# Kernel optimization log

Measured on AMD Instinct MI355X. Metric: run time of the kernel, lower is better.

## Reference

```python
import jax, jax.numpy as jnp
import numpy as np
from math import factorial, sqrt, pi

MUL = 8
LS = [0, 1, 2]                       # l values for both Rs_in and Rs_out
RS = [(MUL, l) for l in LS]
N_NODES = 20000
N_EDGES = 100000
FEAT = sum(m * (2 * l + 1) for m, l in RS)       # 72
R_TOT = sum(mo * mi * (2 * min(lo, li) + 1) for mo, lo in RS for mi, li in RS)  # 1216
L_MAX = max(LS) + max(LS)            # 4
RSH_DIM = (L_MAX + 1) ** 2           # 25
NB, H = 10, 100                      # radial basis size / hidden width
MIN_R, MAX_R = 0.7, 3.2
SWISH_SCALE = 1.679177               # e3nn rescaled swish factor


def _w3j_entry(j1, j2, j3, m1, m2, m3):
    # complex-basis Wigner 3j (Racah formula)
    if m1 + m2 + m3 != 0 or not (abs(j1 - j2) <= j3 <= j1 + j2):
        return 0.0
    t1, t2 = j2 - m1 - j3, j1 + m2 - j3
    kmin, kmax = max(0, t1, t2), min(j1 + j2 - j3, j1 - m1, j2 + m2)
    s = sum((-1) ** k / (factorial(k) * factorial(k - t1) * factorial(k - t2)
                         * factorial(j1 + j2 - j3 - k) * factorial(j1 - m1 - k) * factorial(j2 + m2 - k))
            for k in range(kmin, kmax + 1))
    pref = (-1) ** (j1 - j2 - m3) * sqrt(
        factorial(j1 + j2 - j3) * factorial(j1 - j2 + j3) * factorial(-j1 + j2 + j3) / factorial(j1 + j2 + j3 + 1)
        * factorial(j1 + m1) * factorial(j1 - m1) * factorial(j2 + m2) * factorial(j2 - m2)
        * factorial(j3 + m3) * factorial(j3 - m3))
    return pref * s


def _real_cob(l):
    # complex->real spherical-harmonic change of basis
    U = np.zeros((2 * l + 1, 2 * l + 1), dtype=complex)
    U[l, l] = 1.0
    s = 1.0 / np.sqrt(2.0)
    for m in range(1, l + 1):
        U[l + m, l + m] = (-1) ** m * s
        U[l + m, l - m] = s
        U[l - m, l - m] = 1j * s
        U[l - m, l + m] = -1j * ((-1) ** m) * s
    return U


def _wigner3j_real(l1, l2, l3):
    w = np.zeros((2 * l1 + 1, 2 * l2 + 1, 2 * l3 + 1))
    for m1 in range(-l1, l1 + 1):
        for m2 in range(-l2, l2 + 1):
            m3 = -m1 - m2
            if abs(m3) <= l3:
                w[m1 + l1, m2 + l2, m3 + l3] = _w3j_entry(l1, l2, l3, m1, m2, m3)
    T = np.einsum('am,bn,cp,mnp->abc', _real_cob(l1), _real_cob(l2), _real_cob(l3), w.astype(complex))
    C = T.real if np.linalg.norm(T.real) >= np.linalg.norm(T.imag) else T.imag
    n = np.linalg.norm(C)
    return (C / n if n > 0 else C).astype(np.float32)


# precomputed constants (coupling coefficients + normalization), as in MinimalNetwork.__init__
C3 = {(lo, li, lf): jnp.asarray(_wigner3j_real(lo, li, lf))
      for _, lo in RS for _, li in RS for lf in range(abs(lo - li), lo + li + 1)}


def _norm_coef():
    nc = np.zeros((len(RS), len(RS)), dtype=np.float32)
    for i, (_, lo) in enumerate(RS):
        num = sum(mi * (2 * min(lo, li) + 1) for mi, li in RS)
        nc[i, :] = sqrt(4 * pi) * sqrt(2 * lo + 1) / sqrt(num)
    return jnp.asarray(nc)

NORM = _norm_coef()


def _swish(x):
    return SWISH_SCALE * x * jax.nn.sigmoid(x)


def _radial(r, Ws):
    # GaussianRadialModel: gaussian basis -> 3 hidden swish layers -> linear out
    centers = jnp.linspace(MIN_R, MAX_R, NB)
    sigma = (MAX_R - MIN_R) / (NB - 1)
    x = jnp.exp(-(((r[:, None] - centers) / sigma) ** 2))
    for W in Ws[:-1]:
        x = _swish(x @ (W / jnp.sqrt(jnp.asarray(W.shape[0], x.dtype))))
    W = Ws[-1]
    return x @ (W / jnp.sqrt(jnp.asarray(W.shape[0], x.dtype)))


def _tensor_message(F_src, rsh, R):
    # F_src: [E, FEAT] gathered source features; rsh: [E, 25]; R: [E, R_TOT]
    E = F_src.shape[0]
    f_offs = np.cumsum([0] + [m * (2 * l + 1) for m, l in RS])
    msgs, r_off = [], 0
    for i, (U, lo) in enumerate(RS):
        acc = jnp.zeros((E, U, 2 * lo + 1), F_src.dtype)
        for j, (V, li) in enumerate(RS):
            nlf = 2 * min(lo, li) + 1
            Rb = R[:, r_off:r_off + U * V * nlf].reshape(E, U, V, nlf)
            r_off += U * V * nlf
            Fb = F_src[:, f_offs[j]:f_offs[j + 1]].reshape(E, V, 2 * li + 1)
            for fi, lf in enumerate(range(abs(lo - li), lo + li + 1)):
                # K[e,mo,mi] = sum_mf C3[mo,mi,mf] * Y_lf[e,mf]
                K = jnp.einsum('oif,ef->eoi', C3[(lo, li, lf)], rsh[:, lf * lf:(lf + 1) * (lf + 1)])
                acc = acc + NORM[i, j] * jnp.einsum('eoi,evi,euv->euo', K, Fb, Rb[..., fi])
        msgs.append(acc.reshape(E, -1))
    return jnp.concatenate(msgs, axis=-1)


def _forward(features, edge_index, radii, rsh, Ws):
    R = _radial(radii, Ws)                                     # [E, R_TOT]
    msg = _tensor_message(features[edge_index[0]], rsh, R)     # [E, FEAT]
    # scatter-add aggregation at target nodes (MessagePassing aggr='add')
    return jnp.zeros((features.shape[0], msg.shape[1]), msg.dtype).at[edge_index[1]].add(msg)


def setup_inputs() -> dict:
    key = jax.random.key(0)
    ks = jax.random.split(key, 8)
    features = jax.random.normal(ks[0], (N_NODES, FEAT), jnp.float32)
    edge_index = jax.random.randint(ks[1], (2, N_EDGES), 0, N_NODES)
    radii = MIN_R + (MAX_R - MIN_R) * jax.random.uniform(ks[2], (N_EDGES,), jnp.float32)
    rsh = jax.random.normal(ks[3], (N_EDGES, RSH_DIM), jnp.float32)
    W0 = jax.random.normal(ks[4], (NB, H), jnp.float32)
    W1 = jax.random.normal(ks[5], (H, H), jnp.float32)
    W2 = jax.random.normal(ks[6], (H, H), jnp.float32)
    W3 = jax.random.normal(ks[7], (H, R_TOT), jnp.float32)
    return {"features": features, "edge_index": edge_index, "radii": radii, "rsh": rsh,
            "W0": W0, "W1": W1, "W2": W2, "W3": W3}


def reference(features, edge_index, radii, rsh, W0, W1, W2, W3):
    return _forward(features, edge_index, radii, rsh, (W0, W1, W2, W3))
```

## Files before the change

### kernel.cpp

```cpp
#include <hip/hip_runtime.h>
#include <hip/hip_bf16.h>
#include <math.h>


#define FEATD 72
#define NCOL 1216
#define SWISH_SCALE 1.679177f

typedef __attribute__((ext_vector_type(8))) short bf16x8;
typedef __attribute__((ext_vector_type(4))) float f32x4;

constexpr int NCOMBO = 19;
constexpr int CB_LO[NCOMBO] = {0,0,0,1,1,1,1,1,1,1,2,2,2,2,2,2,2,2,2};
constexpr int CB_LI[NCOMBO] = {0,1,2,0,1,1,1,2,2,2,0,1,1,1,2,2,2,2,2};
constexpr int CB_LF[NCOMBO] = {0,1,2,1,0,1,2,1,2,3,2,1,2,3,0,1,2,3,4};
constexpr int CB_OFF[NCOMBO] = {0,1,10,35,44,53,80,125,170,245,350,375,420,495,600,625,700,825,1000};
constexpr int CB_SZ[NCOMBO]  = {1,9,25,9,9,27,45,45,75,105,25,45,75,105,25,75,125,175,225};
constexpr int C3TOT = 1225;

constexpr int C3OFFT[3][3][5] = {
  { {0,-1,-1,-1,-1}, {-1,1,-1,-1,-1}, {-1,-1,10,-1,-1} },
  { {-1,35,-1,-1,-1}, {44,53,80,-1,-1}, {-1,125,170,245,-1} },
  { {-1,-1,350,-1,-1}, {-1,375,420,495,-1}, {600,625,700,825,1000} }
};
constexpr int ROFFT[3][3] = {{0,64,128},{192,256,448},{640,704,896}};
constexpr int FOFFT[3]   = {0,8,32};

__device__ const double d_fact[11] = {1.,1.,2.,6.,24.,120.,720.,5040.,40320.,362880.,3628800.};

__device__ double w3j_entry(int j1,int j2,int j3,int m1,int m2,int m3){
  if (m1+m2+m3 != 0) return 0.0;
  int dj = j1-j2; if (dj<0) dj=-dj;
  if (j3 < dj || j3 > j1+j2) return 0.0;
  int t1 = j2 - m1 - j3, t2 = j1 + m2 - j3;
  int kmin = 0; if (t1>kmin) kmin=t1; if (t2>kmin) kmin=t2;
  int kmax = j1+j2-j3; if (j1-m1<kmax) kmax=j1-m1; if (j2+m2<kmax) kmax=j2+m2;
  double s = 0.0;
  for (int k=kmin;k<=kmax;++k){
    double den = d_fact[k]*d_fact[k-t1]*d_fact[k-t2]*d_fact[j1+j2-j3-k]
               * d_fact[j1-m1-k]*d_fact[j2+m2-k];
    s += ((k&1)? -1.0:1.0)/den;
  }
  double pref = sqrt(d_fact[j1+j2-j3]*d_fact[j1-j2+j3]*d_fact[-j1+j2+j3]/d_fact[j1+j2+j3+1]
               * d_fact[j1+m1]*d_fact[j1-m1]*d_fact[j2+m2]*d_fact[j2-m2]
               * d_fact[j3+m3]*d_fact[j3-m3]);
  int ex = j1-j2-m3;
  if (ex & 1) pref = -pref;
  return pref*s;
}

__device__ void cob(int l, int r, int c, double& re, double& im){
  re = 0.0; im = 0.0;
  int mr = r - l, mc = c - l;
  const double s = 0.70710678118654752440;
  if (mr == 0) { if (mc == 0) re = 1.0; return; }
  if (mr > 0) {
    if (mc == mr)       re = (mr & 1) ? -s : s;
    else if (mc == -mr) re = s;
  } else {
    int m = -mr;
    if (mc == -m)      im = s;
    else if (mc == m)  im = (m & 1) ? s : -s;
  }
}

__global__ void c3_combined_kernel(float* __restrict__ C3f){
  __shared__ double sre[225], sim[225];
  const int c = blockIdx.x;
  const int lo = CB_LO[c], li = CB_LI[c], lf = CB_LF[c];
  const int off = CB_OFF[c], sz = CB_SZ[c];
  const int n2 = 2*li+1, n3 = 2*lf+1;
  const int t = threadIdx.x;

  for (int p=t; p<sz; p+=64){
    int a = p/(n2*n3), b = (p/n3)%n2, g = p%n3;
    double re=0.0, im=0.0;
    for (int m1=-lo; m1<=lo; ++m1){
      for (int m2=-li; m2<=li; ++m2){
        int m3 = -m1-m2;
        if (m3 < -lf || m3 > lf) continue;
        double w = w3j_entry(lo,li,lf,m1,m2,m3);
        if (w == 0.0) continue;
        double r1,i1,r2,i2,r3,i3;
        cob(lo, a, m1+lo, r1,i1);
        cob(li, b, m2+li, r2,i2);
        cob(lf, g, m3+lf, r3,i3);
        double rr = r1*r2 - i1*i2, ri = r1*i2 + i1*r2;
        double fr = rr*r3 - ri*i3, fi = rr*i3 + ri*r3;
        re += fr*w; im += fi*w;
      }
    }
    sre[p] = re; sim[p] = im;
  }
  __syncthreads();
  double s2r=0.0, s2i=0.0;
  for (int p=t; p<sz; p+=64){ double x=sre[p], y=sim[p]; s2r+=x*x; s2i+=y*y; }
  for (int m=1; m<64; m<<=1){ s2r += __shfl_xor(s2r, m, 64); s2i += __shfl_xor(s2i, m, 64); }
  bool useRe = (s2r >= s2i);
  double n = sqrt(useRe ? s2r : s2i);
  double inv = (n > 0.0) ? 1.0/n : 1.0;
  for (int p=t; p<sz; p+=64){
    double v = useRe ? sre[p] : sim[p];
    C3f[off+p] = (float)(v*inv);
  }
}

__global__ __launch_bounds__(256) void prep_combined_kernel(
    const float* __restrict__ W3, const float* __restrict__ W1,
    const float* __restrict__ W2, __hip_bfloat16* __restrict__ W3t,
    __hip_bfloat16* __restrict__ W1t, __hip_bfloat16* __restrict__ W2t)
{
  int idx = blockIdx.x*256 + threadIdx.x;
  constexpr int NW3 = 1216*128;
  constexpr int HALF = 112*128;
  if (idx < NW3){
    int cp = idx >> 7, k = idx & 127;
    int chunk = cp >> 6, r = cp & 63;
    int lo = CB_LO[chunk], li = CB_LI[chunk], lf = CB_LF[chunk];
    int lmin = lo<li ? lo : li;
    int nlf = 2*lmin+1;
    int fi = lf - (lo>li ? lo-li : li-lo);
    int c = ROFFT[lo][li] + r*nlf + fi;
    float v = (k < 100) ? 0.1f*W3[(size_t)k*NCOL + c] : 0.f;
    int swz = (r*16 + (k>>3)) ^ (r&7);
    W3t[(size_t)chunk*8192 + swz*8 + (k&7)] = __float2bfloat16(v);
  } else if (idx < NW3 + 2*HALF){
    int r2 = idx - NW3;
    const float* W = (r2 < HALF) ? W1 : W2;
    __hip_bfloat16* Wt = (r2 < HALF) ? W1t : W2t;
    int r = (r2 < HALF) ? r2 : r2 - HALF;
    int o = r >> 7, k = r & 127;
    float v = (o < 100 && k < 100) ? 0.1f*W[k*100+o] : 0.f;
    int swz = (o*16 + (k>>3)) ^ (o&7);
    Wt[swz*8 + (k&7)] = __float2bfloat16(v);
  }
}

__global__ __launch_bounds__(256) void hist_kernel(const int* __restrict__ ei,
                                                   int* __restrict__ deg, int E){
  int e = blockIdx.x*256 + threadIdx.x;
  if (e < E) atomicAdd(&deg[ei[E+e]], 1);
}

__global__ __launch_bounds__(256) void scan_kernel(const int* __restrict__ deg,
                                                   int* __restrict__ off,
                                                   int* __restrict__ cursor, int N, int E){
  __shared__ int part[256], spref[256];
  const int t = threadIdx.x;
  const int CH = (N + 255)/256;
  int lo = t*CH, hi = lo+CH < N ? lo+CH : N;
  int s = 0;
  for (int n=lo; n<hi; ++n) s += deg[n];
  part[t] = s;
  __syncthreads();
  if (t == 0){
    int run = 0;
    for (int i=0;i<256;++i){ spref[i] = run; run += part[i]; }
  }
  __syncthreads();
  int run = spref[t];
  for (int n=lo; n<hi; ++n){ off[n] = run; cursor[n] = run; run += deg[n]; }
  if (t == 255) off[N] = E;
}

__global__ __launch_bounds__(256) void fill_kernel(const int* __restrict__ ei,
                                                   int* __restrict__ cursor,
                                                   int* __restrict__ eid, int E){
  int e = blockIdx.x*256 + threadIdx.x;
  if (e < E){
    int idx = atomicAdd(&cursor[ei[E+e]], 1);
    eid[idx] = e;
  }
}

__global__ __launch_bounds__(64) void gather_kernel(const float* __restrict__ msg,
                                                    const int* __restrict__ off,
                                                    const int* __restrict__ eid,
                                                    float* __restrict__ out, int N){
  const int n = blockIdx.x;
  const int t = threadIdx.x;
  const int s = off[n], e1 = off[n+1];
  float a0 = 0.f, a1 = 0.f;
  for (int i=s; i<e1; ++i){
    const float* m = msg + (size_t)eid[i]*FEATD;
    a0 += m[t];
    if (t < 8) a1 += m[64+t];
  }
  out[(size_t)n*FEATD + t] = a0;
  if (t < 8) out[(size_t)n*FEATD + 64 + t] = a1;
}

constexpr int OF_W   = 0;
constexpr int OF_RT  = 16384;
constexpr int OF_ACC = 33792;
constexpr int OF_F   = 44032;
constexpr int OF_KV  = 63488;
constexpr int OF_C3  = 76288;
constexpr int OF_SRC = 81188;
constexpr int SMEM_SZ = 81444;

constexpr int OF_RW   = 0;
constexpr int OF_BAS  = 28672;
constexpr int OF_HA   = 31232;
constexpr int OF_HB   = 48640;

__device__ __forceinline__ float swishf(float s){
  return SWISH_SCALE * s / (1.f + __expf(-s));
}

__device__ __forceinline__ void stage_w(const __hip_bfloat16* __restrict__ Wt,
                                        char* sW, int t)
{
  const int lane = t & 63, wv = t >> 6;
  const char* g = (const char*)Wt;
  #pragma unroll
  for (int i=0; i<7; ++i){
    const char* gsrc = g + (i*256 + wv*64 + lane)*16;
    __builtin_amdgcn_global_load_lds(
        (const __attribute__((address_space(1))) unsigned int*)gsrc,
        (__attribute__((address_space(3))) unsigned int*)(sW + i*4096 + wv*1024),
        16, 0, 0);
  }
}

__device__ __forceinline__ void radial_layer_lds(
    const __hip_bfloat16* __restrict__ sIn,
    const char* __restrict__ sW,
    __hip_bfloat16* __restrict__ sOut,
    int wv, int lr, int lq)
{
  bf16x8 bf[4];
  #pragma unroll
  for (int ks=0; ks<4; ++ks)
    bf[ks] = *(const bf16x8*)&sIn[(wv*16+lr)*136 + ks*32 + lq*8];
  f32x4 acc[7] = {};
  #pragma unroll
  for (int ks=0; ks<4; ++ks)
    #pragma unroll
    for (int ot=0; ot<7; ++ot){
      const int row = ot*16 + lr;
      const int u = (row*16 + ks*4 + lq) ^ (row & 7);
      bf16x8 a = *(const bf16x8*)(sW + u*16);
      acc[ot] = __builtin_amdgcn_mfma_f32_16x16x32_bf16(a, bf[ks], acc[ot], 0, 0, 0);
    }
  #pragma unroll
  for (int ot=0; ot<7; ++ot){
    __hip_bfloat16 hv[4];
    #pragma unroll
    for (int r=0; r<4; ++r)
      hv[r] = __float2bfloat16(swishf(acc[ot][r]));
    *(short4*)&sOut[(wv*16+lr)*136 + ot*16 + lq*4] = *(short4*)hv;
  }
  {
    int lane = lq*16 + lr;
    int row = lane & 15, q = lane >> 4;
    short4 z = {0,0,0,0};
    *(short4*)&sOut[(wv*16+row)*136 + 112 + q*4] = z;
  }
}

__device__ __forceinline__ void stage_chunk(const __hip_bfloat16* __restrict__ W3t,
                                            int chunk, char* sW, int t)
{
  const int lane = t & 63, wv = t >> 6;
  const char* g = (const char*)W3t + (size_t)chunk*16384;
  #pragma unroll
  for (int r=0; r<4; ++r){
    const char* gsrc = g + (wv*256 + r*64 + lane)*16;
    __builtin_amdgcn_global_load_lds(
        (const __attribute__((address_space(1))) unsigned int*)gsrc,
        (__attribute__((address_space(3))) unsigned int*)(sW + wv*4096 + r*1024),
        16, 0, 0);
  }
}

template<int LO,int LI,int LF>
__device__ __forceinline__ void kv_sec(float* kvb, const float* sC3,
                                       const float* __restrict__ rshrow,
                                       int e, int role)
{
  constexpr int NO = 2*LO+1, NI = 2*LI+1, NF = 2*LF+1;
  constexpr int C3B = C3OFFT[LO][LI][LF];
  float y[NF];
  #pragma unroll
  for (int mf=0; mf<NF; ++mf) y[mf] = rshrow[LF*LF + mf];
  for (int it = role; it < NO*NI; it += 4){
    float s = 0.f;
    #pragma unroll
    for (int mf=0; mf<NF; ++mf) s += sC3[C3B + it*NF + mf] * y[mf];
    kvb[e*25 + it] = s;
  }
}

template<int LO,int LI>
__device__ __forceinline__ void consume_sec(
    const float* sRt, const float* sFf, const float* kvb, float* sAcc,
    int e, int role)
{
  constexpr int NO = 2*LO+1, NI = 2*LI+1;
  constexpr int FO = FOFFT[LI];
  float H[2][NI];
  #pragma unroll
  for (int du=0; du<2; ++du)
    #pragma unroll
    for (int mi=0; mi<NI; ++mi) H[du][mi] = 0.f;

  #pragma unroll
  for (int vg=0; vg<2; ++vg){
    float fb[4*NI];
    #pragma unroll
    for (int p=0; p<NI; ++p)
      *(f32x4*)&fb[p*4] = *(const f32x4*)&sFf[e*76 + FO + vg*4*NI + p*4];
    #pragma unroll
    for (int du=0; du<2; ++du){
      const int u = role*2 + du;
      f32x4 rv = *(const f32x4*)&sRt[e*68 + u*8 + vg*4];
      #pragma unroll
      for (int v=0; v<4; ++v)
        #pragma unroll
        for (int mi=0; mi<NI; ++mi)
          H[du][mi] += rv[v] * fb[v*NI + mi];
    }
  }
  const int u0 = role*2, u1 = role*2 + 1;
  const int b0 = e*40 + ((LO==0) ? u0 : (LO==1) ? u0*3 : u0*5);
  const int b1 = e*40 + ((LO==0) ? u1 : (LO==1) ? u1*3 : u1*5);
  #pragma unroll
  for (int o=0; o<NO; ++o){
    float s0 = 0.f, s1 = 0.f;
    #pragma unroll
    for (int mi=0; mi<NI; ++mi){
      float kvv = kvb[e*25 + o*NI + mi];
      s0 += kvv * H[0][mi];
      s1 += kvv * H[1][mi];
    }
    sAcc[b0 + o] += s0;
    sAcc[b1 + o] += s1;
  }
}

__device__ __forceinline__ void mfma_sec(const char* sW, float* sRt,
                                         const bf16x8 (&hf)[4],
                                         int wv, int lr, int lq)
{
  f32x4 a4[4] = {};
  #pragma unroll
  for (int ks=0; ks<4; ++ks){
    #pragma unroll
    for (int ct=0; ct<4; ++ct){
      const int row = ct*16 + lr;
      const int u   = (row*16 + (ks*4 + lq)) ^ (row & 7);
      bf16x8 a = *(const bf16x8*)(sW + u*16);
      a4[ct] = __builtin_amdgcn_mfma_f32_16x16x32_bf16(a, hf[ks], a4[ct], 0, 0, 0);
    }
  }
  #pragma unroll
  for (int ct=0; ct<4; ++ct)
    *(f32x4*)&sRt[(wv*16 + lr)*68 + ct*16 + lq*4] = a4[ct];
}

template<int J0,int W>
__device__ __forceinline__ void flush_group(float* sAcc, float* __restrict__ msg,
                                            int eb, int t, float nrm)
{
  const int lane = t & 63, wv = t >> 6;
  __builtin_amdgcn_wave_barrier();
  for (int p = lane; p < 16*W; p += 64){
    int el = wv*16 + p/W, j = p%W;
    msg[(size_t)(eb + el)*FEATD + J0 + j] = nrm * sAcc[el*40 + j];
    sAcc[el*40 + j] = 0.f;
  }
  __builtin_amdgcn_wave_barrier();
}

template<int LO,int LI,int LF,int PLO,int PLI,int PFLUSH,int CUR>
__device__ __forceinline__ void phase_pl(
    int chunk, const __hip_bfloat16* __restrict__ W3t, const bf16x8 (&hf)[4],
    char* sW, float* sRt, float* sFf, float* sKV, const float* sC3,
    const float* __restrict__ rshrow, float* sAcc,
    float* __restrict__ msg, int eb, int t)
{
  const int e = t >> 2, role = t & 3;
  const int lane = t & 63, wv = t >> 6;
  const int lr = lane & 15, lq = lane >> 4;

  __syncthreads();
  stage_chunk(W3t, chunk, sW, t);

  kv_sec<LO,LI,LF>(sKV + CUR*1600, sC3, rshrow, e, role);
  if constexpr (PLO >= 0)
    consume_sec<PLO,PLI>(sRt, sFf, sKV + (1-CUR)*1600, sAcc, e, role);
  if constexpr (PFLUSH == 0)
    flush_group<0,8>(sAcc, msg, eb, t, 0.72360125f);
  if constexpr (PFLUSH == 1)
    flush_group<8,24>(sAcc, msg, eb, t, 0.8204867f);

  __syncthreads();
  mfma_sec(sW, sRt, hf, wv, lr, lq);
  __builtin_amdgcn_wave_barrier();
}

__global__ __launch_bounds__(256,2) void fused_kernel(
    const float* __restrict__ feats, const int* __restrict__ ei,
    const float* __restrict__ radii, const float* __restrict__ rsh,
    const float* __restrict__ W0,
    const __hip_bfloat16* __restrict__ W1t, const __hip_bfloat16* __restrict__ W2t,
    const __hip_bfloat16* __restrict__ W3t, const float* __restrict__ C3g,
    float* __restrict__ msg, int E)
{
  __shared__ __align__(16) char smem[SMEM_SZ];
  char*  sW   = smem + OF_W;
  float* sRt  = (float*)(smem + OF_RT);
  float* sAcc = (float*)(smem + OF_ACC);
  float* sFf  = (float*)(smem + OF_F);
  float* sKV  = (float*)(smem + OF_KV);
  float* sC3  = (float*)(smem + OF_C3);
  int*   sSrc = (int*)(smem + OF_SRC);
  char*  sWr  = smem + OF_RW;
  float* sbas = (float*)(smem + OF_BAS);
  __hip_bfloat16* hA = (__hip_bfloat16*)(smem + OF_HA);
  __hip_bfloat16* hB = (__hip_bfloat16*)(smem + OF_HB);

  const int t = threadIdx.x;
  const int eb = blockIdx.x*64;
  const int lane = t & 63, wv = t >> 6;
  const int lr = lane & 15, lq = lane >> 4;

  stage_w(W1t, sWr, t);

  for (int p=t; p<640; p+=256){
    int er = p/10, k = p%10;
    int eg = eb + er;
    float r = (eg < E) ? radii[eg] : 0.f;
    float c = 0.7f + (2.5f/9.0f)*(float)k;
    float d = (r - c) * (9.0f/2.5f);
    sbas[p] = __expf(-d*d);
  }
  __syncthreads();
  for (int p=t; p<6400; p+=256){
    int er = p/100, o = p%100;
    float s = 0.f;
    #pragma unroll
    for (int k=0;k<10;++k) s += sbas[er*10+k]*W0[k*100+o];
    hA[er*136+o] = __float2bfloat16(swishf(s*0.3162277660168379f));
  }
  for (int p=t; p<64*36; p+=256){
    int er = p/36, k = 100 + p%36;
    hA[er*136+k] = __float2bfloat16(0.f);
  }
  __syncthreads();

  radial_layer_lds(hA, sWr, hB, wv, lr, lq);
  __syncthreads();
  stage_w(W2t, sWr, t);
  __syncthreads();
  radial_layer_lds(hB, sWr, hA, wv, lr, lq);
  __builtin_amdgcn_wave_barrier();

  bf16x8 hf[4];
  #pragma unroll
  for (int ks=0; ks<4; ++ks)
    hf[ks] = *(const bf16x8*)&hA[(wv*16+lr)*136 + ks*32 + lq*8];

  __syncthreads();

  for (int p=t; p<2560; p+=256) sAcc[p] = 0.f;
  for (int p=t; p<64; p+=256){
    int e = eb + p;
    sSrc[p] = (e < E) ? ei[e] : 0;
  }
  for (int p=t; p<C3TOT; p+=256) sC3[p] = C3g[p];
  __syncthreads();
  for (int p=t; p<64*72; p+=256){
    int el = p/72, j = p%72;
    sFf[el*76 + j] = feats[(size_t)sSrc[el]*72 + j];
  }
  __syncthreads();

  int eg = eb + (t >> 2); if (eg > E-1) eg = E-1;
  const float* rshrow = rsh + (size_t)eg*25;

  phase_pl<0,0,0, -1,-1, -1, 0>( 0, W3t, hf, sW, sRt, sFf, sKV, sC3, rshrow, sAcc, msg, eb, t);
  phase_pl<0,1,1,  0, 0, -1, 1>( 1, W3t, hf, sW, sRt, sFf, sKV, sC3, rshrow, sAcc, msg, eb, t);
  phase_pl<0,2,2,  0, 1, -1, 0>( 2, W3t, hf, sW, sRt, sFf, sKV, sC3, rshrow, sAcc, msg, eb, t);
  phase_pl<1,0,1,  0, 2,  0, 1>( 3, W3t, hf, sW, sRt, sFf, sKV, sC3, rshrow, sAcc, msg, eb, t);
  phase_pl<1,1,0,  1, 0, -1, 0>( 4, W3t, hf, sW, sRt, sFf, sKV, sC3, rshrow, sAcc, msg, eb, t);
  phase_pl<1,1,1,  1, 1, -1, 1>( 5, W3t, hf, sW, sRt, sFf, sKV, sC3, rshrow, sAcc, msg, eb, t);
  phase_pl<1,1,2,  1, 1, -1, 0>( 6, W3t, hf, sW, sRt, sFf, sKV, sC3, rshrow, sAcc, msg, eb, t);
  phase_pl<1,2,1,  1, 1, -1, 1>( 7, W3t, hf, sW, sRt, sFf, sKV, sC3, rshrow, sAcc, msg, eb, t);
  phase_pl<1,2,2,  1, 2, -1, 0>( 8, W3t, hf, sW, sRt, sFf, sKV, sC3, rshrow, sAcc, msg, eb, t);
  phase_pl<1,2,3,  1, 2, -1, 1>( 9, W3t, hf, sW, sRt, sFf, sKV, sC3, rshrow, sAcc, msg, eb, t);
  phase_pl<2,0,2,  1, 2,  1, 0>(10, W3t, hf, sW, sRt, sFf, sKV, sC3, rshrow, sAcc, msg, eb, t);
  phase_pl<2,1,1,  2, 0, -1, 1>(11, W3t, hf, sW, sRt, sFf, sKV, sC3, rshrow, sAcc, msg, eb, t);
  phase_pl<2,1,2,  2, 1, -1, 0>(12, W3t, hf, sW, sRt, sFf, sKV, sC3, rshrow, sAcc, msg, eb, t);
  phase_pl<2,1,3,  2, 1, -1, 1>(13, W3t, hf, sW, sRt, sFf, sKV, sC3, rshrow, sAcc, msg, eb, t);
  phase_pl<2,2,0,  2, 1, -1, 0>(14, W3t, hf, sW, sRt, sFf, sKV, sC3, rshrow, sAcc, msg, eb, t);
  phase_pl<2,2,1,  2, 2, -1, 1>(15, W3t, hf, sW, sRt, sFf, sKV, sC3, rshrow, sAcc, msg, eb, t);
  phase_pl<2,2,2,  2, 2, -1, 0>(16, W3t, hf, sW, sRt, sFf, sKV, sC3, rshrow, sAcc, msg, eb, t);
  phase_pl<2,2,3,  2, 2, -1, 1>(17, W3t, hf, sW, sRt, sFf, sKV, sC3, rshrow, sAcc, msg, eb, t);
  phase_pl<2,2,4,  2, 2, -1, 0>(18, W3t, hf, sW, sRt, sFf, sKV, sC3, rshrow, sAcc, msg, eb, t);

  {
    const int e = t >> 2, role = t & 3;
    consume_sec<2,2>(sRt, sFf, sKV + 0*1600, sAcc, e, role);
    flush_group<32,40>(sAcc, msg, eb, t, 0.9341652f);
  }
}

extern "C" void kernel_launch(void* const* d_in, const int* in_sizes, int n_in,
                              void* d_out, int out_size, void* d_ws, size_t ws_size,
                              hipStream_t stream)
{
  const float* feats = (const float*)d_in[0];
  const int*   ei    = (const int*)d_in[1];
  const float* radii = (const float*)d_in[2];
  const float* rsh   = (const float*)d_in[3];
  const float* W0    = (const float*)d_in[4];
  const float* W1    = (const float*)d_in[5];
  const float* W2    = (const float*)d_in[6];
  const float* W3    = (const float*)d_in[7];
  float* out = (float*)d_out;
  const int E = in_sizes[2];
  const int N = in_sizes[0]/FEATD;

  const int EPAD = ((E + 63)/64)*64;
  const int NBLK = EPAD/64;

  char* ws = (char*)d_ws;
  size_t off_b = 0;
  float*  C3f = (float*)(ws + off_b);  off_b += 8192;
  __hip_bfloat16* W3t = (__hip_bfloat16*)(ws + off_b); off_b += 335872;
  __hip_bfloat16* W1t = (__hip_bfloat16*)(ws + off_b); off_b += 30720;
  __hip_bfloat16* W2t = (__hip_bfloat16*)(ws + off_b); off_b += 30720;
  float* msg = (float*)(ws + off_b);   off_b += (size_t)EPAD*FEATD*4;
  int* deg    = (int*)(ws + off_b);    off_b += (size_t)N*4;
  int* offv   = (int*)(ws + off_b);    off_b += (size_t)(N+1)*4;
  int* cursor = (int*)(ws + off_b);    off_b += (size_t)N*4;
  int* eid    = (int*)(ws + off_b);    off_b += (size_t)E*4;

  c3_combined_kernel<<<dim3(NCOMBO), dim3(64), 0, stream>>>(C3f);
  prep_combined_kernel<<<dim3((1216*128 + 2*112*128 + 255)/256), dim3(256), 0, stream>>>(
      W3, W1, W2, W3t, W1t, W2t);

  hipMemsetAsync(deg, 0, (size_t)N*4, stream);
  hist_kernel<<<dim3((E+255)/256), dim3(256), 0, stream>>>(ei, deg, E);
  scan_kernel<<<dim3(1), dim3(256), 0, stream>>>(deg, offv, cursor, N, E);
  fill_kernel<<<dim3((E+255)/256), dim3(256), 0, stream>>>(ei, cursor, eid, E);

  fused_kernel<<<dim3(NBLK), dim3(256), 0, stream>>>(
      feats, ei, radii, rsh, W0, W1t, W2t, W3t, C3f, msg, E);
  gather_kernel<<<dim3(N), dim3(64), 0, stream>>>(msg, offv, eid, out, N);
}
```

Measured before the change: 405.3 us.

## Replace CSR gather aggregation with direct atomic scatter-add from fused kernel

```diff
diff --git a/kernel.cpp b/kernel.cpp
--- a/kernel.cpp
+++ b/kernel.cpp
@@ -136,60 +136,6 @@
   }
 }
 
-__global__ __launch_bounds__(256) void hist_kernel(const int* __restrict__ ei,
-                                                   int* __restrict__ deg, int E){
-  int e = blockIdx.x*256 + threadIdx.x;
-  if (e < E) atomicAdd(&deg[ei[E+e]], 1);
-}
-
-__global__ __launch_bounds__(256) void scan_kernel(const int* __restrict__ deg,
-                                                   int* __restrict__ off,
-                                                   int* __restrict__ cursor, int N, int E){
-  __shared__ int part[256], spref[256];
-  const int t = threadIdx.x;
-  const int CH = (N + 255)/256;
-  int lo = t*CH, hi = lo+CH < N ? lo+CH : N;
-  int s = 0;
-  for (int n=lo; n<hi; ++n) s += deg[n];
-  part[t] = s;
-  __syncthreads();
-  if (t == 0){
-    int run = 0;
-    for (int i=0;i<256;++i){ spref[i] = run; run += part[i]; }
-  }
-  __syncthreads();
-  int run = spref[t];
-  for (int n=lo; n<hi; ++n){ off[n] = run; cursor[n] = run; run += deg[n]; }
-  if (t == 255) off[N] = E;
-}
-
-__global__ __launch_bounds__(256) void fill_kernel(const int* __restrict__ ei,
-                                                   int* __restrict__ cursor,
-                                                   int* __restrict__ eid, int E){
-  int e = blockIdx.x*256 + threadIdx.x;
-  if (e < E){
-    int idx = atomicAdd(&cursor[ei[E+e]], 1);
-    eid[idx] = e;
-  }
-}
-
-__global__ __launch_bounds__(64) void gather_kernel(const float* __restrict__ msg,
-                                                    const int* __restrict__ off,
-                                                    const int* __restrict__ eid,
-                                                    float* __restrict__ out, int N){
-  const int n = blockIdx.x;
-  const int t = threadIdx.x;
-  const int s = off[n], e1 = off[n+1];
-  float a0 = 0.f, a1 = 0.f;
-  for (int i=s; i<e1; ++i){
-    const float* m = msg + (size_t)eid[i]*FEATD;
-    a0 += m[t];
-    if (t < 8) a1 += m[64+t];
-  }
-  out[(size_t)n*FEATD + t] = a0;
-  if (t < 8) out[(size_t)n*FEATD + 64 + t] = a1;
-}
-
 constexpr int OF_W   = 0;
 constexpr int OF_RT  = 16384;
 constexpr int OF_ACC = 33792;
@@ -197,7 +143,8 @@
 constexpr int OF_KV  = 63488;
 constexpr int OF_C3  = 76288;
 constexpr int OF_SRC = 81188;
-constexpr int SMEM_SZ = 81444;
+constexpr int OF_TGT = 81444;
+constexpr int SMEM_SZ = 81700;
 
 constexpr int OF_RW   = 0;
 constexpr int OF_BAS  = 28672;
@@ -360,14 +307,16 @@
 }
 
 template<int J0,int W>
-__device__ __forceinline__ void flush_group(float* sAcc, float* __restrict__ msg,
-                                            int eb, int t, float nrm)
+__device__ __forceinline__ void flush_group(float* sAcc, float* __restrict__ out,
+                                            const int* sTgt, int eb, int t,
+                                            float nrm, int E)
 {
   const int lane = t & 63, wv = t >> 6;
   __builtin_amdgcn_wave_barrier();
   for (int p = lane; p < 16*W; p += 64){
     int el = wv*16 + p/W, j = p%W;
-    msg[(size_t)(eb + el)*FEATD + J0 + j] = nrm * sAcc[el*40 + j];
+    if (eb + el < E)
+      atomicAdd(&out[(size_t)sTgt[el]*FEATD + J0 + j], nrm * sAcc[el*40 + j]);
     sAcc[el*40 + j] = 0.f;
   }
   __builtin_amdgcn_wave_barrier();
@@ -378,7 +327,7 @@
     int chunk, const __hip_bfloat16* __restrict__ W3t, const bf16x8 (&hf)[4],
     char* sW, float* sRt, float* sFf, float* sKV, const float* sC3,
     const float* __restrict__ rshrow, float* sAcc,
-    float* __restrict__ msg, int eb, int t)
+    float* __restrict__ out, const int* sTgt, int eb, int t, int E)
 {
   const int e = t >> 2, role = t & 3;
   const int lane = t & 63, wv = t >> 6;
@@ -391,9 +340,9 @@
   if constexpr (PLO >= 0)
     consume_sec<PLO,PLI>(sRt, sFf, sKV + (1-CUR)*1600, sAcc, e, role);
   if constexpr (PFLUSH == 0)
-    flush_group<0,8>(sAcc, msg, eb, t, 0.72360125f);
+    flush_group<0,8>(sAcc, out, sTgt, eb, t, 0.72360125f, E);
   if constexpr (PFLUSH == 1)
-    flush_group<8,24>(sAcc, msg, eb, t, 0.8204867f);
+    flush_group<8,24>(sAcc, out, sTgt, eb, t, 0.8204867f, E);
 
   __syncthreads();
   mfma_sec(sW, sRt, hf, wv, lr, lq);
@@ -406,7 +355,7 @@
     const float* __restrict__ W0,
     const __hip_bfloat16* __restrict__ W1t, const __hip_bfloat16* __restrict__ W2t,
     const __hip_bfloat16* __restrict__ W3t, const float* __restrict__ C3g,
-    float* __restrict__ msg, int E)
+    float* __restrict__ out, int E)
 {
   __shared__ __align__(16) char smem[SMEM_SZ];
   char*  sW   = smem + OF_W;
@@ -416,6 +365,7 @@
   float* sKV  = (float*)(smem + OF_KV);
   float* sC3  = (float*)(smem + OF_C3);
   int*   sSrc = (int*)(smem + OF_SRC);
+  int*   sTgt = (int*)(smem + OF_TGT);
   char*  sWr  = smem + OF_RW;
   float* sbas = (float*)(smem + OF_BAS);
   __hip_bfloat16* hA = (__hip_bfloat16*)(smem + OF_HA);
@@ -468,6 +418,7 @@
   for (int p=t; p<64; p+=256){
     int e = eb + p;
     sSrc[p] = (e < E) ? ei[e] : 0;
+    sTgt[p] = (e < E) ? ei[E + e] : 0;
   }
   for (int p=t; p<C3TOT; p+=256) sC3[p] = C3g[p];
   __syncthreads();
@@ -480,30 +431,30 @@
   int eg = eb + (t >> 2); if (eg > E-1) eg = E-1;
   const float* rshrow = rsh + (size_t)eg*25;
 
-  phase_pl<0,0,0, -1,-1, -1, 0>( 0, W3t, hf, sW, sRt, sFf, sKV, sC3, rshrow, sAcc, msg, eb, t);
-  phase_pl<0,1,1,  0, 0, -1, 1>( 1, W3t, hf, sW, sRt, sFf, sKV, sC3, rshrow, sAcc, msg, eb, t);
-  phase_pl<0,2,2,  0, 1, -1, 0>( 2, W3t, hf, sW, sRt, sFf, sKV, sC3, rshrow, sAcc, msg, eb, t);
-  phase_pl<1,0,1,  0, 2,  0, 1>( 3, W3t, hf, sW, sRt, sFf, sKV, sC3, rshrow, sAcc, msg, eb, t);
-  phase_pl<1,1,0,  1, 0, -1, 0>( 4, W3t, hf, sW, sRt, sFf, sKV, sC3, rshrow, sAcc, msg, eb, t);
-  phase_pl<1,1,1,  1, 1, -1, 1>( 5, W3t, hf, sW, sRt, sFf, sKV, sC3, rshrow, sAcc, msg, eb, t);
-  phase_pl<1,1,2,  1, 1, -1, 0>( 6, W3t, hf, sW, sRt, sFf, sKV, sC3, rshrow, sAcc, msg, eb, t);
-  phase_pl<1,2,1,  1, 1, -1, 1>( 7, W3t, hf, sW, sRt, sFf, sKV, sC3, rshrow, sAcc, msg, eb, t);
-  phase_pl<1,2,2,  1, 2, -1, 0>( 8, W3t, hf, sW, sRt, sFf, sKV, sC3, rshrow, sAcc, msg, eb, t);
-  phase_pl<1,2,3,  1, 2, -1, 1>( 9, W3t, hf, sW, sRt, sFf, sKV, sC3, rshrow, sAcc, msg, eb, t);
-  phase_pl<2,0,2,  1, 2,  1, 0>(10, W3t, hf, sW, sRt, sFf, sKV, sC3, rshrow, sAcc, msg, eb, t);
-  phase_pl<2,1,1,  2, 0, -1, 1>(11, W3t, hf, sW, sRt, sFf, sKV, sC3, rshrow, sAcc, msg, eb, t);
-  phase_pl<2,1,2,  2, 1, -1, 0>(12, W3t, hf, sW, sRt, sFf, sKV, sC3, rshrow, sAcc, msg, eb, t);
-  phase_pl<2,1,3,  2, 1, -1, 1>(13, W3t, hf, sW, sRt, sFf, sKV, sC3, rshrow, sAcc, msg, eb, t);
-  phase_pl<2,2,0,  2, 1, -1, 0>(14, W3t, hf, sW, sRt, sFf, sKV, sC3, rshrow, sAcc, msg, eb, t);
-  phase_pl<2,2,1,  2, 2, -1, 1>(15, W3t, hf, sW, sRt, sFf, sKV, sC3, rshrow, sAcc, msg, eb, t);
-  phase_pl<2,2,2,  2, 2, -1, 0>(16, W3t, hf, sW, sRt, sFf, sKV, sC3, rshrow, sAcc, msg, eb, t);
-  phase_pl<2,2,3,  2, 2, -1, 1>(17, W3t, hf, sW, sRt, sFf, sKV, sC3, rshrow, sAcc, msg, eb, t);
-  phase_pl<2,2,4,  2, 2, -1, 0>(18, W3t, hf, sW, sRt, sFf, sKV, sC3, rshrow, sAcc, msg, eb, t);
+  phase_pl<0,0,0, -1,-1, -1, 0>( 0, W3t, hf, sW, sRt, sFf, sKV, sC3, rshrow, sAcc, out, sTgt, eb, t, E);
+  phase_pl<0,1,1,  0, 0, -1, 1>( 1, W3t, hf, sW, sRt, sFf, sKV, sC3, rshrow, sAcc, out, sTgt, eb, t, E);
+  phase_pl<0,2,2,  0, 1, -1, 0>( 2, W3t, hf, sW, sRt, sFf, sKV, sC3, rshrow, sAcc, out, sTgt, eb, t, E);
+  phase_pl<1,0,1,  0, 2,  0, 1>( 3, W3t, hf, sW, sRt, sFf, sKV, sC3, rshrow, sAcc, out, sTgt, eb, t, E);
+  phase_pl<1,1,0,  1, 0, -1, 0>( 4, W3t, hf, sW, sRt, sFf, sKV, sC3, rshrow, sAcc, out, sTgt, eb, t, E);
+  phase_pl<1,1,1,  1, 1, -1, 1>( 5, W3t, hf, sW, sRt, sFf, sKV, sC3, rshrow, sAcc, out, sTgt, eb, t, E);
+  phase_pl<1,1,2,  1, 1, -1, 0>( 6, W3t, hf, sW, sRt, sFf, sKV, sC3, rshrow, sAcc, out, sTgt, eb, t, E);
+  phase_pl<1,2,1,  1, 1, -1, 1>( 7, W3t, hf, sW, sRt, sFf, sKV, sC3, rshrow, sAcc, out, sTgt, eb, t, E);
+  phase_pl<1,2,2,  1, 2, -1, 0>( 8, W3t, hf, sW, sRt, sFf, sKV, sC3, rshrow, sAcc, out, sTgt, eb, t, E);
+  phase_pl<1,2,3,  1, 2, -1, 1>( 9, W3t, hf, sW, sRt, sFf, sKV, sC3, rshrow, sAcc, out, sTgt, eb, t, E);
+  phase_pl<2,0,2,  1, 2,  1, 0>(10, W3t, hf, sW, sRt, sFf, sKV, sC3, rshrow, sAcc, out, sTgt, eb, t, E);
+  phase_pl<2,1,1,  2, 0, -1, 1>(11, W3t, hf, sW, sRt, sFf, sKV, sC3, rshrow, sAcc, out, sTgt, eb, t, E);
+  phase_pl<2,1,2,  2, 1, -1, 0>(12, W3t, hf, sW, sRt, sFf, sKV, sC3, rshrow, sAcc, out, sTgt, eb, t, E);
+  phase_pl<2,1,3,  2, 1, -1, 1>(13, W3t, hf, sW, sRt, sFf, sKV, sC3, rshrow, sAcc, out, sTgt, eb, t, E);
+  phase_pl<2,2,0,  2, 1, -1, 0>(14, W3t, hf, sW, sRt, sFf, sKV, sC3, rshrow, sAcc, out, sTgt, eb, t, E);
+  phase_pl<2,2,1,  2, 2, -1, 1>(15, W3t, hf, sW, sRt, sFf, sKV, sC3, rshrow, sAcc, out, sTgt, eb, t, E);
+  phase_pl<2,2,2,  2, 2, -1, 0>(16, W3t, hf, sW, sRt, sFf, sKV, sC3, rshrow, sAcc, out, sTgt, eb, t, E);
+  phase_pl<2,2,3,  2, 2, -1, 1>(17, W3t, hf, sW, sRt, sFf, sKV, sC3, rshrow, sAcc, out, sTgt, eb, t, E);
+  phase_pl<2,2,4,  2, 2, -1, 0>(18, W3t, hf, sW, sRt, sFf, sKV, sC3, rshrow, sAcc, out, sTgt, eb, t, E);
 
   {
     const int e = t >> 2, role = t & 3;
     consume_sec<2,2>(sRt, sFf, sKV + 0*1600, sAcc, e, role);
-    flush_group<32,40>(sAcc, msg, eb, t, 0.9341652f);
+    flush_group<32,40>(sAcc, out, sTgt, eb, t, 0.9341652f, E);
   }
 }
 
@@ -521,7 +472,6 @@
   const float* W3    = (const float*)d_in[7];
   float* out = (float*)d_out;
   const int E = in_sizes[2];
-  const int N = in_sizes[0]/FEATD;
 
   const int EPAD = ((E + 63)/64)*64;
   const int NBLK = EPAD/64;
@@ -532,22 +482,13 @@
   __hip_bfloat16* W3t = (__hip_bfloat16*)(ws + off_b); off_b += 335872;
   __hip_bfloat16* W1t = (__hip_bfloat16*)(ws + off_b); off_b += 30720;
   __hip_bfloat16* W2t = (__hip_bfloat16*)(ws + off_b); off_b += 30720;
-  float* msg = (float*)(ws + off_b);   off_b += (size_t)EPAD*FEATD*4;
-  int* deg    = (int*)(ws + off_b);    off_b += (size_t)N*4;
-  int* offv   = (int*)(ws + off_b);    off_b += (size_t)(N+1)*4;
-  int* cursor = (int*)(ws + off_b);    off_b += (size_t)N*4;
-  int* eid    = (int*)(ws + off_b);    off_b += (size_t)E*4;
+
+  hipMemsetAsync(out, 0, (size_t)out_size*sizeof(float), stream);
 
   c3_combined_kernel<<<dim3(NCOMBO), dim3(64), 0, stream>>>(C3f);
   prep_combined_kernel<<<dim3((1216*128 + 2*112*128 + 255)/256), dim3(256), 0, stream>>>(
       W3, W1, W2, W3t, W1t, W2t);
 
-  hipMemsetAsync(deg, 0, (size_t)N*4, stream);
-  hist_kernel<<<dim3((E+255)/256), dim3(256), 0, stream>>>(ei, deg, E);
-  scan_kernel<<<dim3(1), dim3(256), 0, stream>>>(deg, offv, cursor, N, E);
-  fill_kernel<<<dim3((E+255)/256), dim3(256), 0, stream>>>(ei, cursor, eid, E);
-
   fused_kernel<<<dim3(NBLK), dim3(256), 0, stream>>>(
-      feats, ei, radii, rsh, W0, W1t, W2t, W3t, C3f, msg, E);
-  gather_kernel<<<dim3(N), dim3(64), 0, stream>>>(msg, offv, eid, out, N);
-}
+      feats, ei, radii, rsh, W0, W1t, W2t, W3t, C3f, out, E);
+}
```

Result: faster. 340.8 us (-15.9%).
